# Performance work log

Hardware: AMD Instinct MI355X
Metric: run time of the kernel (lower is better)

The kernel has to match this reference:

```python
import jax, jax.numpy as jnp
import numpy as np

B, S, V, D, H, NL, FF, MAXD, OUTLEN, NC = 8, 1024, 64, 512, 8, 6, 2048, 64, 8, 10
HD = D // H


def _layernorm(x, g, b, eps=1e-5):
    m = jnp.mean(x, axis=-1, keepdims=True)
    v = jnp.var(x, axis=-1, keepdims=True)
    return (x - m) * jax.lax.rsqrt(v + eps) * g + b


def setup_inputs() -> dict:
    key = jax.random.key(0)
    ks = jax.random.split(key, 24)
    s = 0.02
    inp = {
        'src': jax.random.randint(ks[0], (B, S), 0, V, dtype=jnp.int32),
        'src_pad_mask': jnp.zeros((B, S), dtype=bool),
        'embed': jax.random.normal(ks[1], (V, D), jnp.float32) * s,
        'cls_token': jnp.zeros((D,), jnp.float32),
        'qkv_w': jax.random.normal(ks[2], (NL, 3 * D, D), jnp.float32) * s,
        'qkv_b': jnp.zeros((NL, 3 * D), jnp.float32),
        'out_w': jax.random.normal(ks[3], (NL, D, D), jnp.float32) * s,
        'out_b': jnp.zeros((NL, D), jnp.float32),
        'rel_emb': jax.random.normal(ks[4], (NL, 2 * MAXD + 1, H), jnp.float32) * s,
        'ln1_g': jnp.ones((NL, D), jnp.float32),
        'ln1_b': jnp.zeros((NL, D), jnp.float32),
        'w1': jax.random.normal(ks[5], (NL, FF, D), jnp.float32) * s,
        'b1': jnp.zeros((NL, FF), jnp.float32),
        'w2': jax.random.normal(ks[6], (NL, D, FF), jnp.float32) * s,
        'b2': jnp.zeros((NL, D), jnp.float32),
        'ln2_g': jnp.ones((NL, D), jnp.float32),
        'ln2_b': jnp.zeros((NL, D), jnp.float32),
        'norm_g': jnp.ones((D,), jnp.float32),
        'norm_b': jnp.zeros((D,), jnp.float32),
        'cls_w': jax.random.normal(ks[7], (OUTLEN * NC, D), jnp.float32) * s,
        'cls_b': jnp.zeros((OUTLEN * NC,), jnp.float32),
    }
    return inp


def _forward(src, src_pad_mask, embed, cls_token, qkv_w, qkv_b, out_w, out_b,
             rel_emb, ln1_g, ln1_b, w1, b1, w2, b2, ln2_g, ln2_b,
             norm_g, norm_b, cls_w, cls_b):
    b = src.shape[0]
    x = embed[src]                                         # [B,S,D]
    cls = jnp.broadcast_to(cls_token, (b, 1, D))
    x = jnp.concatenate([cls, x], axis=1)                  # [B,L,D], L=S+1
    L = x.shape[1]
    full_mask = jnp.concatenate([jnp.zeros((b, 1), bool), src_pad_mask], axis=1)

    # relative position indices, shared across layers
    rel = jnp.arange(L)[None, :] - jnp.arange(L)[:, None]  # [L,L]
    maxd = (rel_emb.shape[1] - 1) // 2
    rel = jnp.clip(rel, -maxd, maxd) + maxd
    scale = HD ** -0.5
    neg = jnp.asarray(-1e9, x.dtype)

    def layer(x, p):
        (qw, qb, ow, ob, re, g1, be1, W1, B1, W2, B2, g2, be2) = p
        qkv = jnp.einsum('bld,ed->ble', x, qw) + qb        # [B,L,3D]
        q, k, v = jnp.split(qkv, 3, axis=-1)
        q = q.reshape(b, L, H, HD)
        k = k.reshape(b, L, H, HD)
        v = v.reshape(b, L, H, HD)
        scores = jnp.einsum('bqhd,bkhd->bhqk', q, k) * scale
        bias = re[rel]                                     # [L,L,H]
        scores = scores + jnp.transpose(bias, (2, 0, 1))[None]
        scores = jnp.where(full_mask[:, None, None, :], neg, scores)
        attn = jax.nn.softmax(scores, axis=-1)
        o = jnp.einsum('bhqk,bkhd->bqhd', attn, v).reshape(b, L, D)
        o = jnp.einsum('bld,ed->ble', o, ow) + ob
        x2 = _layernorm(x + o, g1, be1)
        h = jax.nn.gelu(jnp.einsum('bld,fd->blf', x2, W1) + B1, approximate=False)
        ff = jnp.einsum('blf,df->bld', h, W2) + B2
        x3 = _layernorm(x2 + ff, g2, be2)
        return x3, None

    xs = (qkv_w, qkv_b, out_w, out_b, rel_emb, ln1_g, ln1_b,
          w1, b1, w2, b2, ln2_g, ln2_b)
    x, _ = jax.lax.scan(layer, x, xs)
    x = _layernorm(x, norm_g, norm_b)
    cls_repr = x[:, 0, :]
    logits = jnp.einsum('bd,od->bo', cls_repr, cls_w) + cls_b
    return logits.reshape(b, OUTLEN, NC)


def reference(src, src_pad_mask, embed, cls_token, qkv_w, qkv_b, out_w, out_b,
              rel_emb, ln1_g, ln1_b, w1, b1, w2, b2, ln2_g, ln2_b,
              norm_g, norm_b, cls_w, cls_b):
    return _forward(src, src_pad_mask, embed, cls_token, qkv_w, qkv_b, out_w,
                    out_b, rel_emb, ln1_g, ln1_b, w1, b1, w2, b2, ln2_g,
                    ln2_b, norm_g, norm_b, cls_w, cls_b)
```

## Files before the change

### kernel.cpp

```cpp
#include <hip/hip_runtime.h>
#include <hip/hip_bf16.h>
#include <stdint.h>

#define B 8
#define S 1024
#define L 1025
#define D 512
#define H 8
#define HD 64
#define NL 6
#define FF 2048
#define MAXD 64
#define OUTLEN 8
#define NC 10

#define MP 8320

typedef __bf16 bf16;
typedef __bf16 bf16x8 __attribute__((ext_vector_type(8)));
typedef __bf16 bf16x4 __attribute__((ext_vector_type(4)));
typedef float f32x4 __attribute__((ext_vector_type(4)));

__device__ __forceinline__ float fexp2(float x) { return __builtin_amdgcn_exp2f(x); }

#define LGKM_BARRIER() asm volatile("s_waitcnt lgkmcnt(0)\ns_barrier" ::: "memory")

__device__ __forceinline__ void gld16(const void* g, void* l) {
    __builtin_amdgcn_global_load_lds(
        (const __attribute__((address_space(1))) unsigned int*)g,
        (__attribute__((address_space(3))) unsigned int*)l,
        16, 0, 0);
}

__device__ __forceinline__ float fast_gelu(float v) {
    float x = v * 0.70710678118654752f;
    float ax = fabsf(x);
    float t = 1.f / fmaf(0.3275911f, ax, 1.f);
    float poly = t * (0.254829592f + t * (-0.284496736f + t * (1.421413741f +
                 t * (-1.453152027f + t * 1.061405429f))));
    float e = fexp2(-ax * ax * 1.4426950408889634f);
    float erfv = 1.f - poly * e;
    erfv = copysignf(erfv, x);
    return 0.5f * v * (1.f + erfv);
}

__global__ __launch_bounds__(256) void cvt_k(const float* __restrict__ in,
                                             bf16* __restrict__ out, int n4)
{
    int i = blockIdx.x * 256 + threadIdx.x;
    if (i >= n4) return;
    float4 v = reinterpret_cast<const float4*>(in)[i];
    bf16x4 o;
    o[0] = (bf16)v.x; o[1] = (bf16)v.y; o[2] = (bf16)v.z; o[3] = (bf16)v.w;
    reinterpret_cast<bf16x4*>(out)[i] = o;
}

__global__ void embed_k(const int* __restrict__ src, const float* __restrict__ emb,
                        const float* __restrict__ cls, float* __restrict__ x,
                        bf16* __restrict__ xb)
{
    long i = (long)blockIdx.x * blockDim.x + threadIdx.x;
    if (i >= (long)B * L * D) return;
    int d = (int)(i % D);
    long bl = i / D;
    int l = (int)(bl % L);
    int b = (int)(bl / L);
    float v = (l == 0) ? cls[d] : emb[(long)src[b * S + (l - 1)] * D + d];
    x[i] = v;
    xb[i] = (bf16)v;
}

template<int ACT, int OBF, int BIAS, int RT>
__global__ __launch_bounds__(256) void mgemm(const bf16* __restrict__ A,
                                             const bf16* __restrict__ W,
                                             const float* __restrict__ bias,
                                             float* __restrict__ Cf,
                                             bf16* __restrict__ Cb,
                                             int N, int K, int LDA)
{
    __shared__ bf16 Asl[3][RT * 32];
    __shared__ bf16 Bsl[3][128 * 32];
    int tid = threadIdx.x;
    int m0 = blockIdx.y * RT;
    int n0 = blockIdx.x * 128;
    int lane = tid & 63;
    int w = tid >> 6;
    int wbase = tid & ~63;
    int kb = (lane >> 4) * 8;
    int rsel = lane & 15;
    constexpr int FJ = (RT == 128) ? 4 : 2;
    constexpr int CW = (RT == 128) ? 64 : 32;
    int wr, wc;
    if constexpr (RT == 128) { wr = w >> 1; wc = w & 1; }
    else                     { wr = 0;      wc = w;     }
    f32x4 acc[4][FJ] = {};

    auto stage = [&](int buf, int k0) {
        if constexpr (RT == 128) {
#pragma unroll
            for (int r = 0; r < 2; r++) {
                int s = r * 256 + tid;
                int sb = r * 256 + wbase;
                gld16(A + (size_t)(m0 + (s >> 2)) * LDA + k0 + (s & 3) * 8, &Asl[buf][(size_t)sb * 8]);
                gld16(W + (size_t)(n0 + (s >> 2)) * LDA + k0 + (s & 3) * 8, &Bsl[buf][(size_t)sb * 8]);
            }
        } else {
            gld16(A + (size_t)(m0 + (tid >> 2)) * LDA + k0 + (tid & 3) * 8, &Asl[buf][(size_t)wbase * 8]);
#pragma unroll
            for (int r = 0; r < 2; r++) {
                int s = r * 256 + tid;
                int sb = r * 256 + wbase;
                gld16(W + (size_t)(n0 + (s >> 2)) * LDA + k0 + (s & 3) * 8, &Bsl[buf][(size_t)sb * 8]);
            }
        }
    };

    stage(0, 0);
    if (32 < K) stage(1, 32);

    int cur = 0;
    for (int k0 = 0; k0 < K; k0 += 32) {
        if constexpr (RT == 128)
            asm volatile("s_waitcnt vmcnt(4)\ns_barrier" ::: "memory");
        else
            asm volatile("s_waitcnt vmcnt(3)\ns_barrier" ::: "memory");
        int b2 = cur + 2; if (b2 >= 3) b2 -= 3;
        if (k0 + 64 < K) stage(b2, k0 + 64);

        bf16x8 af[4], bfr[FJ];
#pragma unroll
        for (int fi = 0; fi < 4; fi++)
            af[fi] = *reinterpret_cast<const bf16x8*>(&Asl[cur][(wr * 64 + fi * 16 + rsel) * 32 + kb]);
#pragma unroll
        for (int fj = 0; fj < FJ; fj++)
            bfr[fj] = *reinterpret_cast<const bf16x8*>(&Bsl[cur][(wc * CW + fj * 16 + rsel) * 32 + kb]);
#pragma unroll
        for (int fi = 0; fi < 4; fi++)
#pragma unroll
            for (int fj = 0; fj < FJ; fj++)
                acc[fi][fj] = __builtin_amdgcn_mfma_f32_16x16x32_bf16(af[fi], bfr[fj], acc[fi][fj], 0, 0, 0);
        cur = (cur + 1 == 3) ? 0 : cur + 1;
    }
    int rowb = (lane >> 4) * 4;
    int colb = lane & 15;
#pragma unroll
    for (int fi = 0; fi < 4; fi++) {
#pragma unroll
        for (int fj = 0; fj < FJ; fj++) {
            int col = n0 + wc * CW + fj * 16 + colb;
            float bsv = BIAS ? bias[col] : 0.f;
#pragma unroll
            for (int i = 0; i < 4; i++) {
                int row = m0 + wr * 64 + fi * 16 + rowb + i;
                float v = acc[fi][fj][i] + bsv;
                if (ACT) v = fast_gelu(v);
                if (OBF) Cb[(size_t)row * N + col] = (bf16)v;
                else     Cf[(size_t)row * N + col] = v;
            }
        }
    }
}

__global__ __launch_bounds__(256) void fattn_k(const bf16* __restrict__ qkv,
                                               const float* __restrict__ rel_emb_l,
                                               const unsigned char* __restrict__ pad,
                                               bf16* __restrict__ ob)
{
    constexpr int PIT = 72;
    __shared__ bf16 Vt[2][64 * PIT];
    __shared__ bf16 Psh[4][2][16 * PIT];
    __shared__ float bias2s[2 * MAXD + 1];
    __shared__ float colm[2][64];

    const int bh = blockIdx.x;
    const int qt = blockIdx.y;
    const int h = bh & 7, b = bh >> 3;
    const int q0 = qt * 128;
    const int tid = threadIdx.x;
    const int lane = tid & 63;
    const int w = tid >> 6;
    const int ln15 = lane & 15, g4 = lane >> 4;
    const int kb8 = g4 * 8;
    constexpr float LOG2E = 1.4426950408889634f;
    constexpr float C2 = 0.125f * LOG2E;

    const char* base = (const char*)qkv + (size_t)(b * L) * 3072 + (size_t)h * (HD * 2);

    for (int i = tid; i < 2 * MAXD + 1; i += 256) bias2s[i] = rel_emb_l[i * H + h] * LOG2E;
    if (tid < 64) colm[0][tid] = (tid > 0 && pad[(size_t)b * S + tid - 1]) ? -1e9f : 0.f;

    int qrow[2];
    bf16x8 qa[2][2];
#pragma unroll
    for (int qq = 0; qq < 2; qq++) {
        qrow[qq] = q0 + qq * 64 + w * 16 + ln15;
        qa[qq][0] = *(const bf16x8*)(base + (size_t)qrow[qq] * 3072 + g4 * 16);
        qa[qq][1] = *(const bf16x8*)(base + (size_t)qrow[qq] * 3072 + 64 + g4 * 16);
    }

    const int vr = tid >> 3;
    const int vd0 = (tid & 7) * 8;
    const int vsw = ((vd0 >> 3) & 7) << 3;

    {
        bf16x8 a = *(const bf16x8*)(base + (size_t)vr * 3072 + 2048 + vd0 * 2);
        bf16x8 c = *(const bf16x8*)(base + (size_t)(vr + 32) * 3072 + 2048 + vd0 * 2);
#pragma unroll
        for (int j = 0; j < 8; j++) {
            Vt[0][(vd0 + j) * PIT + (vr ^ vsw)] = a[j];
            Vt[0][(vd0 + j) * PIT + ((vr + 32) ^ vsw)] = c[j];
        }
    }
    bf16x8 kr[4][2];
#pragma unroll
    for (int fj = 0; fj < 4; fj++) {
        const char* rp = base + (size_t)(fj * 16 + ln15) * 3072 + 1024 + g4 * 16;
        kr[fj][0] = *(const bf16x8*)(rp);
        kr[fj][1] = *(const bf16x8*)(rp + 64);
    }
    LGKM_BARRIER();

    f32x4 oacc[2][4] = {};
    float m_prev[2] = {-1e30f, -1e30f};
    float l_sum[2] = {0.f, 0.f};

    for (int t = 0; t < 17; t++) {
        const int k0 = t * 64;
        const int k0n = (k0 + 64 > 1024) ? 1024 : (k0 + 64);
        const int cur = t & 1;

        bf16x8 vA = *(const bf16x8*)(base + (size_t)(k0n + vr) * 3072 + 2048 + vd0 * 2);
        bf16x8 vB = *(const bf16x8*)(base + (size_t)(k0n + vr + 32) * 3072 + 2048 + vd0 * 2);

        f32x4 sacc[2][4] = {};
#pragma unroll
        for (int qq = 0; qq < 2; qq++)
#pragma unroll
            for (int fj = 0; fj < 4; fj++) {
                sacc[qq][fj] = __builtin_amdgcn_mfma_f32_16x16x32_bf16(kr[fj][0], qa[qq][0], sacc[qq][fj], 0, 0, 0);
                sacc[qq][fj] = __builtin_amdgcn_mfma_f32_16x16x32_bf16(kr[fj][1], qa[qq][1], sacc[qq][fj], 0, 0, 0);
            }
#pragma unroll
        for (int fj = 0; fj < 4; fj++) {
            const char* rp = base + (size_t)(k0n + fj * 16 + ln15) * 3072 + 1024 + g4 * 16;
            kr[fj][0] = *(const bf16x8*)(rp);
            kr[fj][1] = *(const bf16x8*)(rp + 64);
        }

        f32x4 cm[4];
#pragma unroll
        for (int fj = 0; fj < 4; fj++)
            cm[fj] = *(const f32x4*)&colm[cur][fj * 16 + g4 * 4];

#pragma unroll
        for (int qq = 0; qq < 2; qq++) {
            float sv[4][4];
            const int relbw = k0 - q0 - qq * 64 - w * 16;
            if (relbw >= MAXD + 15 || relbw <= -MAXD - 63) {
                const float bu = bias2s[relbw > 0 ? 2 * MAXD : 0];
#pragma unroll
                for (int fj = 0; fj < 4; fj++)
#pragma unroll
                    for (int i = 0; i < 4; i++)
                        sv[fj][i] = fmaf(sacc[qq][fj][i], C2, bu + cm[fj][i]);
            } else {
                const int relb = k0 - qrow[qq];
#pragma unroll
                for (int fj = 0; fj < 4; fj++)
#pragma unroll
                    for (int i = 0; i < 4; i++) {
                        int rel = relb + fj * 16 + g4 * 4 + i;
                        rel = rel < -MAXD ? -MAXD : (rel > MAXD ? MAXD : rel);
                        sv[fj][i] = fmaf(sacc[qq][fj][i], C2, bias2s[rel + MAXD] + cm[fj][i]);
                    }
            }

            float mx = sv[0][0];
#pragma unroll
            for (int fj = 0; fj < 4; fj++)
#pragma unroll
                for (int i = 0; i < 4; i++) mx = fmaxf(mx, sv[fj][i]);
            mx = fmaxf(mx, __shfl_xor(mx, 16));
            mx = fmaxf(mx, __shfl_xor(mx, 32));
            const float mnew = fmaxf(m_prev[qq], mx);
            const float corr = fexp2(m_prev[qq] - mnew);
            float rsum = 0.f;
            float pb[4][4];
#pragma unroll
            for (int fj = 0; fj < 4; fj++)
#pragma unroll
                for (int i = 0; i < 4; i++) {
                    float p = fexp2(sv[fj][i] - mnew);
                    pb[fj][i] = p;
                    rsum += p;
                }
            rsum += __shfl_xor(rsum, 16);
            rsum += __shfl_xor(rsum, 32);
            l_sum[qq] = l_sum[qq] * corr + rsum;
            m_prev[qq] = mnew;
#pragma unroll
            for (int fd = 0; fd < 4; fd++) oacc[qq][fd] *= corr;

#pragma unroll
            for (int fj = 0; fj < 4; fj++) {
                union { bf16 hh[4]; unsigned long long u; } pk;
                pk.hh[0] = (bf16)pb[fj][0]; pk.hh[1] = (bf16)pb[fj][1];
                pk.hh[2] = (bf16)pb[fj][2]; pk.hh[3] = (bf16)pb[fj][3];
                *(unsigned long long*)&Psh[w][qq][ln15 * PIT + fj * 16 + g4 * 4] = pk.u;
            }
        }

#pragma unroll
        for (int j = 0; j < 8; j++) {
            Vt[cur ^ 1][(vd0 + j) * PIT + (vr ^ vsw)] = vA[j];
            Vt[cur ^ 1][(vd0 + j) * PIT + ((vr + 32) ^ vsw)] = vB[j];
        }
        if (tid < 64) {
            int gk = k0 + 64 + tid;
            int pi = (gk <= 1024) ? gk - 1 : 0;
            colm[cur ^ 1][tid] = (gk > 1024 || pad[(size_t)b * S + pi]) ? -1e9f : 0.f;
        }

        LGKM_BARRIER();

        bf16x8 pa[2][2];
#pragma unroll
        for (int qq = 0; qq < 2; qq++) {
            pa[qq][0] = *(const bf16x8*)&Psh[w][qq][ln15 * PIT + kb8];
            pa[qq][1] = *(const bf16x8*)&Psh[w][qq][ln15 * PIT + 32 + kb8];
        }
#pragma unroll
        for (int fd = 0; fd < 4; fd++) {
            const int d = fd * 16 + ln15;
            const int vx = ((d >> 3) & 7) << 3;
            bf16x8 af0 = *(const bf16x8*)&Vt[cur][d * PIT + (kb8 ^ vx)];
            bf16x8 af1 = *(const bf16x8*)&Vt[cur][d * PIT + ((32 + kb8) ^ vx)];
            oacc[0][fd] = __builtin_amdgcn_mfma_f32_16x16x32_bf16(af0, pa[0][0], oacc[0][fd], 0, 0, 0);
            oacc[0][fd] = __builtin_amdgcn_mfma_f32_16x16x32_bf16(af1, pa[0][1], oacc[0][fd], 0, 0, 0);
            oacc[1][fd] = __builtin_amdgcn_mfma_f32_16x16x32_bf16(af0, pa[1][0], oacc[1][fd], 0, 0, 0);
            oacc[1][fd] = __builtin_amdgcn_mfma_f32_16x16x32_bf16(af1, pa[1][1], oacc[1][fd], 0, 0, 0);
        }
        LGKM_BARRIER();
    }

#pragma unroll
    for (int qq = 0; qq < 2; qq++) {
        if (qrow[qq] < L) {
            const float inv = 1.f / l_sum[qq];
            bf16* op = ob + (size_t)(b * L + qrow[qq]) * D + h * HD + g4 * 4;
#pragma unroll
            for (int fd = 0; fd < 4; fd++) {
                bf16x4 r;
#pragma unroll
                for (int i = 0; i < 4; i++) r[i] = (bf16)(oacc[qq][fd][i] * inv);
                *(bf16x4*)(op + fd * 16) = r;
            }
        }
    }
}

__global__ __launch_bounds__(256) void add_ln_k(const float* __restrict__ xin,
                                                const float* __restrict__ rin,
                                                const float* __restrict__ g,
                                                const float* __restrict__ bb,
                                                float* __restrict__ out,
                                                bf16* __restrict__ outb)
{
    int row = blockIdx.x;
    __shared__ float red[8];
    int tid = threadIdx.x;
    const float* xp = xin + (size_t)row * D;
    const float* rp = rin + (size_t)row * D;
    float v0 = xp[tid] + rp[tid];
    float v1 = xp[tid + 256] + rp[tid + 256];
    float s = v0 + v1;
    for (int off = 32; off; off >>= 1) s += __shfl_down(s, off, 64);
    int lane = tid & 63, wid = tid >> 6;
    if (lane == 0) red[wid] = s;
    __syncthreads();
    if (tid == 0) red[0] = red[0] + red[1] + red[2] + red[3];
    __syncthreads();
    float mean = red[0] * (1.f / D);
    float d0 = v0 - mean, d1 = v1 - mean;
    float sq = d0 * d0 + d1 * d1;
    for (int off = 32; off; off >>= 1) sq += __shfl_down(sq, off, 64);
    if (lane == 0) red[4 + wid] = sq;
    __syncthreads();
    if (tid == 0) red[4] = red[4] + red[5] + red[6] + red[7];
    __syncthreads();
    float rs = rsqrtf(red[4] * (1.f / D) + 1e-5f);
    float r0 = d0 * rs * g[tid] + bb[tid];
    float r1 = d1 * rs * g[tid + 256] + bb[tid + 256];
    out[(size_t)row * D + tid] = r0;
    out[(size_t)row * D + tid + 256] = r1;
    outb[(size_t)row * D + tid] = (bf16)r0;
    outb[(size_t)row * D + tid + 256] = (bf16)r1;
}

__global__ __launch_bounds__(256) void cls_k(const float* __restrict__ x,
                                             const float* __restrict__ ng,
                                             const float* __restrict__ nb,
                                             const float* __restrict__ cw,
                                             const float* __restrict__ cb,
                                             float* __restrict__ out)
{
    int b = blockIdx.x;
    __shared__ float xn[D];
    __shared__ float red[8];
    int tid = threadIdx.x;
    const float* xp = x + (size_t)(b * L) * D;
    float v0 = xp[tid], v1 = xp[tid + 256];
    float s = v0 + v1;
    for (int off = 32; off; off >>= 1) s += __shfl_down(s, off, 64);
    int lane = tid & 63, wid = tid >> 6;
    if (lane == 0) red[wid] = s;
    __syncthreads();
    if (tid == 0) red[0] = red[0] + red[1] + red[2] + red[3];
    __syncthreads();
    float mean = red[0] * (1.f / D);
    float d0 = v0 - mean, d1 = v1 - mean;
    float sq = d0 * d0 + d1 * d1;
    for (int off = 32; off; off >>= 1) sq += __shfl_down(sq, off, 64);
    if (lane == 0) red[4 + wid] = sq;
    __syncthreads();
    if (tid == 0) red[4] = red[4] + red[5] + red[6] + red[7];
    __syncthreads();
    float rs = rsqrtf(red[4] * (1.f / D) + 1e-5f);
    xn[tid] = d0 * rs * ng[tid] + nb[tid];
    xn[tid + 256] = d1 * rs * ng[tid + 256] + nb[tid + 256];
    __syncthreads();
    for (int o = tid; o < OUTLEN * NC; o += 256) {
        float acc = cb[o];
        const float* wp = cw + (size_t)o * D;
        for (int d = 0; d < D; d++) acc += xn[d] * wp[d];
        out[b * OUTLEN * NC + o] = acc;
    }
}

extern "C" void kernel_launch(void* const* d_in, const int* in_sizes, int n_in,
                              void* d_out, int out_size, void* d_ws, size_t ws_size,
                              hipStream_t stream) {
    const int* src = (const int*)d_in[0];
    const unsigned char* pad = (const unsigned char*)d_in[1];
    const float* emb = (const float*)d_in[2];
    const float* cls_token = (const float*)d_in[3];
    const float* qkv_w = (const float*)d_in[4];
    const float* qkv_b = (const float*)d_in[5];
    const float* out_w = (const float*)d_in[6];
    const float* out_b = (const float*)d_in[7];
    const float* rel_emb = (const float*)d_in[8];
    const float* ln1_g = (const float*)d_in[9];
    const float* ln1_b = (const float*)d_in[10];
    const float* w1 = (const float*)d_in[11];
    const float* b1 = (const float*)d_in[12];
    const float* w2 = (const float*)d_in[13];
    const float* b2 = (const float*)d_in[14];
    const float* ln2_g = (const float*)d_in[15];
    const float* ln2_b = (const float*)d_in[16];
    const float* norm_g = (const float*)d_in[17];
    const float* norm_b = (const float*)d_in[18];
    const float* cls_w = (const float*)d_in[19];
    const float* cls_b = (const float*)d_in[20];
    float* out = (float*)d_out;

    char* ws = (char*)d_ws;
    size_t off = 0;
    float* x   = (float*)(ws + off); off += (size_t)MP * D * 4;
    bf16*  xb  = (bf16*) (ws + off); off += (size_t)MP * D * 2;
    float* x2  = (float*)(ws + off); off += (size_t)MP * D * 4;
    bf16*  x2b = (bf16*) (ws + off); off += (size_t)MP * D * 2;
    char*  R   = ws + off;           off += (size_t)MP * 3 * D * 4;
    bf16*  qkvb = (bf16*)R;
    bf16*  hb  = (bf16*)R;
    float* p   = (float*)(R + (size_t)MP * FF * 2);
    bf16*  obf = (bf16*) (ws + off); off += (size_t)MP * D * 2;

    const size_t WQ = (size_t)NL * 3 * D * D;
    const size_t WO = (size_t)NL * D * D;
    const size_t W1E = (size_t)NL * FF * D;
    const size_t W2E = (size_t)NL * D * FF;
    const size_t WALL = WQ + WO + W1E + W2E;
    bool all_w = (off + WALL * 2) <= ws_size;

    bf16 *wq_a = nullptr, *wo_a = nullptr, *w1_a = nullptr, *w2_a = nullptr, *wbuf = nullptr;
    if (all_w) {
        wq_a = (bf16*)(ws + off);
        wo_a = wq_a + WQ;
        w1_a = wo_a + WO;
        w2_a = w1_a + W1E;
        int n4;
        n4 = (int)(WQ / 4);  cvt_k<<<dim3((n4 + 255) / 256), 256, 0, stream>>>(qkv_w, wq_a, n4);
        n4 = (int)(WO / 4);  cvt_k<<<dim3((n4 + 255) / 256), 256, 0, stream>>>(out_w, wo_a, n4);
        n4 = (int)(W1E / 4); cvt_k<<<dim3((n4 + 255) / 256), 256, 0, stream>>>(w1, w1_a, n4);
        n4 = (int)(W2E / 4); cvt_k<<<dim3((n4 + 255) / 256), 256, 0, stream>>>(w2, w2_a, n4);
    } else {
        wbuf = (bf16*)(ws + off);
    }

    const int M = B * L;
    {
        long total = (long)B * L * D;
        embed_k<<<dim3((unsigned)((total + 255) / 256)), 256, 0, stream>>>(src, emb, cls_token, x, xb);
    }
    for (int l = 0; l < NL; l++) {
        const float* qb  = qkv_b + (size_t)l * 3 * D;
        const float* obi = out_b + (size_t)l * D;
        const float* re  = rel_emb + (size_t)l * (2 * MAXD + 1) * H;
        const float* g1  = ln1_g + (size_t)l * D;
        const float* be1 = ln1_b + (size_t)l * D;
        const float* B1p = b1 + (size_t)l * FF;
        const float* B2p = b2 + (size_t)l * D;
        const float* g2  = ln2_g + (size_t)l * D;
        const float* be2 = ln2_b + (size_t)l * D;

        const bf16 *wqb, *wob, *w1b, *w2b;
        if (all_w) {
            wqb = wq_a + (size_t)l * 3 * D * D;
            wob = wo_a + (size_t)l * D * D;
            w1b = w1_a + (size_t)l * FF * D;
            w2b = w2_a + (size_t)l * D * FF;
        } else {
            bf16* wp_ = wbuf;
            wqb = wp_;            wp_ += 3 * D * D;
            wob = wp_;            wp_ += D * D;
            w1b = wp_;            wp_ += FF * D;
            w2b = wp_;
            int n4;
            n4 = 3 * D * D / 4; cvt_k<<<dim3((n4 + 255) / 256), 256, 0, stream>>>(qkv_w + (size_t)l * 3 * D * D, (bf16*)wqb, n4);
            n4 = D * D / 4;     cvt_k<<<dim3((n4 + 255) / 256), 256, 0, stream>>>(out_w + (size_t)l * D * D, (bf16*)wob, n4);
            n4 = FF * D / 4;    cvt_k<<<dim3((n4 + 255) / 256), 256, 0, stream>>>(w1 + (size_t)l * FF * D, (bf16*)w1b, n4);
            n4 = D * FF / 4;    cvt_k<<<dim3((n4 + 255) / 256), 256, 0, stream>>>(w2 + (size_t)l * D * FF, (bf16*)w2b, n4);
        }

        mgemm<0, 1, 1, 128><<<dim3(3 * D / 128, MP / 128), 256, 0, stream>>>(xb, wqb, qb, nullptr, qkvb, 3 * D, D, D);
        fattn_k<<<dim3(B * H, 9), 256, 0, stream>>>(qkvb, re, pad, obf);
        mgemm<0, 0, 1, 64><<<dim3(D / 128, MP / 64), 256, 0, stream>>>(obf, wob, obi, p, nullptr, D, D, D);
        add_ln_k<<<dim3(M), 256, 0, stream>>>(x, p, g1, be1, x2, x2b);
        mgemm<1, 1, 1, 128><<<dim3(FF / 128, MP / 128), 256, 0, stream>>>(x2b, w1b, B1p, nullptr, hb, FF, D, D);
        mgemm<0, 0, 1, 64><<<dim3(D / 128, MP / 64), 256, 0, stream>>>(hb, w2b, B2p, p, nullptr, D, FF, FF);
        add_ln_k<<<dim3(M), 256, 0, stream>>>(x2, p, g2, be2, x, xb);
    }
    cls_k<<<dim3(B), 256, 0, stream>>>(x, norm_g, norm_b, cls_w, cls_b, out);
}
```

Baseline: 1.490 ms.

## Fuse out-projection and FFN2 GEMMs with residual add and layernorm

Adds a gemm_ln kernel in which each block computes a 16-row by full-512-column output tile with MFMA. In the epilogue it adds bias and the residual, reduces mean and variance across the row, and writes both fp32 and bf16 normalized outputs. This replaces the two mgemm + add_ln_k pairs per layer, removing the fp32 intermediate buffer round trip and two launches per layer. The cost is that every 16-row block streams the entire weight matrix (up to 512x2048 bf16). That gives poor weight reuse, and a 64KB double-buffered LDS tile limits occupancy. Variance now uses the E[x^2]-mean^2 form.

```diff
diff --git a/kernel.cpp b/kernel.cpp
--- a/kernel.cpp
+++ b/kernel.cpp
@@ -161,6 +161,118 @@
     }
 }
 
+__global__ __launch_bounds__(256) void gemm_ln(const bf16* __restrict__ A,
+                                               const bf16* __restrict__ W,
+                                               const float* __restrict__ bias,
+                                               const float* __restrict__ xres,
+                                               const float* __restrict__ gam,
+                                               const float* __restrict__ bet,
+                                               float* __restrict__ outF,
+                                               bf16* __restrict__ outB,
+                                               int K)
+{
+    __shared__ bf16 Asl[2][16 * 32];
+    __shared__ bf16 Bsl[2][512 * 32];
+    __shared__ float red[2][4][16];
+    int tid = threadIdx.x;
+    int m0 = blockIdx.x * 16;
+    int lane = tid & 63;
+    int w = tid >> 6;
+    int wbase = tid & ~63;
+    int ln15 = lane & 15, g4 = lane >> 4;
+    int kb = g4 * 8;
+    f32x4 acc[8] = {};
+
+    auto stage = [&](int buf, int k0) {
+        if (w == 0)
+            gld16(A + (size_t)(m0 + (tid >> 2)) * K + k0 + (tid & 3) * 8, &Asl[buf][0]);
+#pragma unroll
+        for (int r = 0; r < 8; r++) {
+            int s = r * 256 + tid;
+            gld16(W + (size_t)(s >> 2) * K + k0 + (s & 3) * 8,
+                  &Bsl[buf][(size_t)(r * 256 + wbase) * 8]);
+        }
+    };
+
+    stage(0, 0);
+    __syncthreads();
+
+    for (int k0 = 0; k0 < K; k0 += 32) {
+        int cur = (k0 >> 5) & 1;
+        if (k0 + 32 < K) stage(cur ^ 1, k0 + 32);
+        bf16x8 af = *reinterpret_cast<const bf16x8*>(&Asl[cur][ln15 * 32 + kb]);
+        bf16x8 bfr[8];
+#pragma unroll
+        for (int fj = 0; fj < 8; fj++)
+            bfr[fj] = *reinterpret_cast<const bf16x8*>(&Bsl[cur][(w * 128 + fj * 16 + ln15) * 32 + kb]);
+#pragma unroll
+        for (int fj = 0; fj < 8; fj++)
+            acc[fj] = __builtin_amdgcn_mfma_f32_16x16x32_bf16(af, bfr[fj], acc[fj], 0, 0, 0);
+        __syncthreads();
+    }
+
+    int col[8];
+    float bcol[8], gcol[8], betcol[8];
+#pragma unroll
+    for (int fj = 0; fj < 8; fj++) {
+        col[fj] = w * 128 + fj * 16 + ln15;
+        bcol[fj] = bias[col[fj]];
+        gcol[fj] = gam[col[fj]];
+        betcol[fj] = bet[col[fj]];
+    }
+    f32x4 v[8];
+#pragma unroll
+    for (int fj = 0; fj < 8; fj++) {
+#pragma unroll
+        for (int i = 0; i < 4; i++) {
+            int row = m0 + g4 * 4 + i;
+            v[fj][i] = acc[fj][i] + bcol[fj] + xres[(size_t)row * 512 + col[fj]];
+        }
+    }
+    f32x4 psum = {}, psq = {};
+#pragma unroll
+    for (int fj = 0; fj < 8; fj++) {
+        psum += v[fj];
+        psq += v[fj] * v[fj];
+    }
+#pragma unroll
+    for (int off = 1; off < 16; off <<= 1) {
+#pragma unroll
+        for (int i = 0; i < 4; i++) {
+            psum[i] += __shfl_xor(psum[i], off, 16);
+            psq[i] += __shfl_xor(psq[i], off, 16);
+        }
+    }
+    if (ln15 == 0) {
+#pragma unroll
+        for (int i = 0; i < 4; i++) {
+            red[0][w][g4 * 4 + i] = psum[i];
+            red[1][w][g4 * 4 + i] = psq[i];
+        }
+    }
+    __syncthreads();
+    float mean[4], rs[4];
+#pragma unroll
+    for (int i = 0; i < 4; i++) {
+        int r16 = g4 * 4 + i;
+        float s = red[0][0][r16] + red[0][1][r16] + red[0][2][r16] + red[0][3][r16];
+        float sq = red[1][0][r16] + red[1][1][r16] + red[1][2][r16] + red[1][3][r16];
+        mean[i] = s * (1.f / 512.f);
+        float var = sq * (1.f / 512.f) - mean[i] * mean[i];
+        rs[i] = rsqrtf(var + 1e-5f);
+    }
+#pragma unroll
+    for (int fj = 0; fj < 8; fj++) {
+#pragma unroll
+        for (int i = 0; i < 4; i++) {
+            int row = m0 + g4 * 4 + i;
+            float o = (v[fj][i] - mean[i]) * rs[i] * gcol[fj] + betcol[fj];
+            outF[(size_t)row * 512 + col[fj]] = o;
+            outB[(size_t)row * 512 + col[fj]] = (bf16)o;
+        }
+    }
+}
+
 __global__ __launch_bounds__(256) void fattn_k(const bf16* __restrict__ qkv,
                                                const float* __restrict__ rel_emb_l,
                                                const unsigned char* __restrict__ pad,
@@ -357,44 +469,6 @@
             }
         }
     }
-}
-
-__global__ __launch_bounds__(256) void add_ln_k(const float* __restrict__ xin,
-                                                const float* __restrict__ rin,
-                                                const float* __restrict__ g,
-                                                const float* __restrict__ bb,
-                                                float* __restrict__ out,
-                                                bf16* __restrict__ outb)
-{
-    int row = blockIdx.x;
-    __shared__ float red[8];
-    int tid = threadIdx.x;
-    const float* xp = xin + (size_t)row * D;
-    const float* rp = rin + (size_t)row * D;
-    float v0 = xp[tid] + rp[tid];
-    float v1 = xp[tid + 256] + rp[tid + 256];
-    float s = v0 + v1;
-    for (int off = 32; off; off >>= 1) s += __shfl_down(s, off, 64);
-    int lane = tid & 63, wid = tid >> 6;
-    if (lane == 0) red[wid] = s;
-    __syncthreads();
-    if (tid == 0) red[0] = red[0] + red[1] + red[2] + red[3];
-    __syncthreads();
-    float mean = red[0] * (1.f / D);
-    float d0 = v0 - mean, d1 = v1 - mean;
-    float sq = d0 * d0 + d1 * d1;
-    for (int off = 32; off; off >>= 1) sq += __shfl_down(sq, off, 64);
-    if (lane == 0) red[4 + wid] = sq;
-    __syncthreads();
-    if (tid == 0) red[4] = red[4] + red[5] + red[6] + red[7];
-    __syncthreads();
-    float rs = rsqrtf(red[4] * (1.f / D) + 1e-5f);
-    float r0 = d0 * rs * g[tid] + bb[tid];
-    float r1 = d1 * rs * g[tid + 256] + bb[tid + 256];
-    out[(size_t)row * D + tid] = r0;
-    out[(size_t)row * D + tid + 256] = r1;
-    outb[(size_t)row * D + tid] = (bf16)r0;
-    outb[(size_t)row * D + tid + 256] = (bf16)r1;
 }
 
 __global__ __launch_bounds__(256) void cls_k(const float* __restrict__ x,
@@ -472,7 +546,6 @@
     char*  R   = ws + off;           off += (size_t)MP * 3 * D * 4;
     bf16*  qkvb = (bf16*)R;
     bf16*  hb  = (bf16*)R;
-    float* p   = (float*)(R + (size_t)MP * FF * 2);
     bf16*  obf = (bf16*) (ws + off); off += (size_t)MP * D * 2;
 
     const size_t WQ = (size_t)NL * 3 * D * D;
@@ -497,7 +570,6 @@
         wbuf = (bf16*)(ws + off);
     }
 
-    const int M = B * L;
     {
         long total = (long)B * L * D;
         embed_k<<<dim3((unsigned)((total + 255) / 256)), 256, 0, stream>>>(src, emb, cls_token, x, xb);
@@ -534,11 +606,9 @@
 
         mgemm<0, 1, 1, 128><<<dim3(3 * D / 128, MP / 128), 256, 0, stream>>>(xb, wqb, qb, nullptr, qkvb, 3 * D, D, D);
         fattn_k<<<dim3(B * H, 9), 256, 0, stream>>>(qkvb, re, pad, obf);
-        mgemm<0, 0, 1, 64><<<dim3(D / 128, MP / 64), 256, 0, stream>>>(obf, wob, obi, p, nullptr, D, D, D);
-        add_ln_k<<<dim3(M), 256, 0, stream>>>(x, p, g1, be1, x2, x2b);
+        gemm_ln<<<dim3(MP / 16), 256, 0, stream>>>(obf, wob, obi, x, g1, be1, x2, x2b, D);
         mgemm<1, 1, 1, 128><<<dim3(FF / 128, MP / 128), 256, 0, stream>>>(x2b, w1b, B1p, nullptr, hb, FF, D, D);
-        mgemm<0, 0, 1, 64><<<dim3(D / 128, MP / 64), 256, 0, stream>>>(hb, w2b, B2p, p, nullptr, D, FF, FF);
-        add_ln_k<<<dim3(M), 256, 0, stream>>>(x2, p, g2, be2, x, xb);
+        gemm_ln<<<dim3(MP / 16), 256, 0, stream>>>(hb, w2b, B2p, x2, g2, be2, x, xb, FF);
     }
     cls_k<<<dim3(B), 256, 0, stream>>>(x, norm_g, norm_b, cls_w, cls_b, out);
 }
```

Measured after the change: 1.993 ms. 33.7% more time.
